# Kernel tuning notes

Measured on AMD Instinct MI355X. Metric: run time of the kernel, lower is better.

Reference implementation:

```python
import jax, jax.numpy as jnp
import numpy as np
import math

B, H, N, D = 4, 8, 2048, 64


def setup_inputs() -> dict:
    key = jax.random.key(0)
    kq, kk, kv = jax.random.split(key, 3)
    q = jax.random.normal(kq, (B, H, N, D), dtype=jnp.float32)
    k = jax.random.normal(kk, (B, H, N, D), dtype=jnp.float32)
    v = jax.random.normal(kv, (B, H, N, D), dtype=jnp.float32)
    return {"q": q, "k": k, "v": v}


def reference(q, k, v):
    # global_attention_Sub: expanded squared L2 distance ||q_i - k_j||^2
    # = qq_i - 2 q_i.k_j + kk_j, then softmax(-dist/sqrt(D)) @ v.
    scale = math.sqrt(q.shape[-1])
    inner = -2.0 * jnp.einsum('bhnd,bhmd->bhnm', q, k)          # [B,H,N,N]
    qq = jnp.sum(q * q, axis=-1, keepdims=True)                  # [B,H,N,1]
    kk = jnp.sum(k * k, axis=-1, keepdims=True)                  # [B,H,N,1]
    diff_sq = qq + inner + jnp.swapaxes(kk, -1, -2)              # [B,H,N,N]
    attn = jax.nn.softmax(-diff_sq / scale, axis=-1)
    x = jnp.einsum('bhnm,bhmd->bhnd', attn, v)                   # [B,H,N,D]
    return jnp.transpose(x, (0, 2, 1, 3))                        # [B,N,H,D]
```

## Files before the change

kernel.cpp:

```cpp
#include <hip/hip_runtime.h>

typedef __bf16 bf16x4 __attribute__((ext_vector_type(4)));
typedef __bf16 bf16x8 __attribute__((ext_vector_type(8)));
typedef float floatx4 __attribute__((ext_vector_type(4)));

constexpr int Bc = 4, Hc = 8, Nc = 2048, Dc = 64;
constexpr int BQ = 128;
constexpr int WQ = 32;
constexpr int TK = 64;
constexpr int NT = Nc / TK;
constexpr int SPS = 72;
constexpr float LOG2E = 1.44269504088896340736f;

constexpr size_t KSW_OFF = 0;
constexpr size_t VSW_OFF = (size_t)32 * NT * 8192;
constexpr size_t KKN_OFF = VSW_OFF * 2;

typedef __attribute__((address_space(1))) const unsigned int gu32;
typedef __attribute__((address_space(3))) unsigned int lu32;
__device__ __forceinline__ void dma16(const void* g, void* l) {
    __builtin_amdgcn_global_load_lds((gu32*)g, (lu32*)l, 16, 0, 0);
}
__device__ __forceinline__ void dma4(const void* g, void* l) {
    __builtin_amdgcn_global_load_lds((gu32*)g, (lu32*)l, 4, 0, 0);
}

__global__ __launch_bounds__(256) void prep_kernel(
    const float* __restrict__ Kg, const float* __restrict__ Vg, char* __restrict__ ws)
{
    __shared__ float sT[64 * 68];
    const int tid = threadIdx.x;
    const int jt = blockIdx.x, bh = blockIdx.y;

    __bf16* Ksw = (__bf16*)(ws + KSW_OFF) + ((size_t)bh * NT + jt) * 4096;
    __bf16* Vsw = (__bf16*)(ws + VSW_OFF) + ((size_t)bh * NT + jt) * 4096;
    float*  kkn = (float*)(ws + KKN_OFF) + (size_t)bh * Nc + jt * 64;
    const size_t tb = ((size_t)bh * Nc + jt * 64) * Dc;

#pragma unroll
    for (int cc = 0; cc < 2; ++cc) {
        const int g   = tid + cc * 256;
        const int key = g >> 3, kcx = g & 7;
        const int kc  = kcx ^ (key & 7);
        const float* src = Kg + tb + key * 64 + kc * 8;
        float4 a = *(const float4*)src;
        float4 b = *(const float4*)(src + 4);
        float ss = a.x*a.x + a.y*a.y + a.z*a.z + a.w*a.w
                 + b.x*b.x + b.y*b.y + b.z*b.z + b.w*b.w;
        ss += __shfl_xor(ss, 1);
        ss += __shfl_xor(ss, 2);
        ss += __shfl_xor(ss, 4);
        if (kcx == 0) kkn[key] = -(ss * 0.125f * LOG2E);
        bf16x8 c8;
        c8[0]=(__bf16)a.x; c8[1]=(__bf16)a.y; c8[2]=(__bf16)a.z; c8[3]=(__bf16)a.w;
        c8[4]=(__bf16)b.x; c8[5]=(__bf16)b.y; c8[6]=(__bf16)b.z; c8[7]=(__bf16)b.w;
        *(bf16x8*)(Ksw + g * 8) = c8;
    }
    {
        const int js = tid >> 2, dc = (tid & 3) * 16;
        const float* vr = Vg + tb + js * 64 + dc;
        float* dst = &sT[js * 68 + dc];
        *(float4*)dst       = *(const float4*)vr;
        *(float4*)(dst + 4) = *(const float4*)(vr + 4);
        *(float4*)(dst + 8) = *(const float4*)(vr + 8);
        *(float4*)(dst + 12)= *(const float4*)(vr + 12);
    }
    __syncthreads();
#pragma unroll
    for (int cc = 0; cc < 2; ++cc) {
        const int g = tid + cc * 256;
        const int d = g >> 3, kcx = g & 7;
        const int kc = kcx ^ (d & 7);
        bf16x8 c8;
#pragma unroll
        for (int e = 0; e < 8; ++e) {
            const int ee = (e + kcx) & 7;
            c8[ee] = (__bf16)sT[(kc * 8 + ee) * 68 + d];
        }
        *(bf16x8*)(Vsw + g * 8) = c8;
    }
}

__global__ __launch_bounds__(256, 2) void attn_kernel(
    const float* __restrict__ Qg, const char* __restrict__ ws, float* __restrict__ Og)
{
    __shared__ __align__(16) __bf16 sK[2][4096];
    __shared__ __align__(16) __bf16 sVall[3 * 4096];
    __shared__ __align__(16) float  skk[2][64];
    __shared__ __align__(16) __bf16 sP[BQ * SPS];
    __shared__ __align__(16) float  sl[BQ];

    const int tid  = threadIdx.x;
    const int wave = tid >> 6;
    const int lane = tid & 63;
    const int qd   = lane >> 4;
    const int c    = lane & 15;

    const int qt = blockIdx.x;
    const int bh = blockIdx.y;

    const char* Kimg = ws + KSW_OFF + (size_t)bh * NT * 8192;
    const char* Vimg = ws + VSW_OFF + (size_t)bh * NT * 8192;
    const float* kkp = (const float*)(ws + KKN_OFF) + (size_t)bh * Nc;

    const float qscale = 0.25f * LOG2E;
    const int i0 = qt * BQ + wave * WQ;

    bf16x8 qf[2][2];
#pragma unroll
    for (int h = 0; h < 2; ++h) {
        const float* qrow = Qg + ((size_t)bh * Nc + i0 + h * 16 + c) * Dc + qd * 8;
#pragma unroll
        for (int ks = 0; ks < 2; ++ks) {
            float4 a = *(const float4*)(qrow + ks * 32);
            float4 b = *(const float4*)(qrow + ks * 32 + 4);
            bf16x8 f;
            f[0] = (__bf16)(a.x * qscale); f[1] = (__bf16)(a.y * qscale);
            f[2] = (__bf16)(a.z * qscale); f[3] = (__bf16)(a.w * qscale);
            f[4] = (__bf16)(b.x * qscale); f[5] = (__bf16)(b.y * qscale);
            f[6] = (__bf16)(b.z * qscale); f[7] = (__bf16)(b.w * qscale);
            qf[h][ks] = f;
        }
    }

    const int koff0 = c * 64 + ((qd ^ (c & 7)) << 3);
    const int koff1 = c * 64 + (((4 + qd) ^ (c & 7)) << 3);

    floatx4 oacc[2][4];
#pragma unroll
    for (int h = 0; h < 2; ++h)
#pragma unroll
        for (int dt = 0; dt < 4; ++dt)
#pragma unroll
            for (int e = 0; e < 4; ++e) oacc[h][dt][e] = 0.f;
    float lp[2] = {0.f, 0.f};

    __bf16* vprev = &sVall[2 * 4096];
    __bf16* vcur  = &sVall[0];
    __bf16* vnext = &sVall[1 * 4096];

    auto stage = [&](int jt2, int kb, __bf16* vdst) {
        const char* ki = Kimg + (size_t)jt2 * 8192;
        const char* vi = Vimg + (size_t)jt2 * 8192;
#pragma unroll
        for (int i = 0; i < 2; ++i) {
            const int off    = wave * 2048 + i * 1024 + lane * 16;
            const int ldsoff = wave * 2048 + i * 1024;
            dma16(ki + off, (char*)&sK[kb][0] + ldsoff);
            dma16(vi + off, (char*)vdst + ldsoff);
        }
        if (wave == 3) dma4(kkp + jt2 * 64 + lane, &skk[kb][0]);
    };

    stage(0, 0, vcur);

    bf16x8 pfp[2][2];

    for (int jt = 0; jt < NT; ++jt) {
        const int b = jt & 1;
        __syncthreads();
        if (jt + 1 < NT) stage(jt + 1, b ^ 1, vnext);

        floatx4 st[2][4];
#pragma unroll
        for (int kt = 0; kt < 4; ++kt) {
            floatx4 kkf = *(const floatx4*)&skk[b][kt * 16 + qd * 4];
            st[0][kt] = kkf; st[1][kt] = kkf;
        }
#pragma unroll
        for (int kt = 0; kt < 4; ++kt) {
            const __bf16* kbase = &sK[b][kt * 1024];
            bf16x8 kf0 = *(const bf16x8*)(kbase + koff0);
            bf16x8 kf1 = *(const bf16x8*)(kbase + koff1);
            st[0][kt] = __builtin_amdgcn_mfma_f32_16x16x32_bf16(kf0, qf[0][0], st[0][kt], 0, 0, 0);
            st[0][kt] = __builtin_amdgcn_mfma_f32_16x16x32_bf16(kf1, qf[0][1], st[0][kt], 0, 0, 0);
            st[1][kt] = __builtin_amdgcn_mfma_f32_16x16x32_bf16(kf0, qf[1][0], st[1][kt], 0, 0, 0);
            st[1][kt] = __builtin_amdgcn_mfma_f32_16x16x32_bf16(kf1, qf[1][1], st[1][kt], 0, 0, 0);
        }

        if (jt > 0) {
#pragma unroll
            for (int dt = 0; dt < 4; ++dt) {
                const __bf16* vbase = vprev + dt * 1024;
                bf16x8 vf0 = *(const bf16x8*)(vbase + koff0);
                bf16x8 vf1 = *(const bf16x8*)(vbase + koff1);
                oacc[0][dt] = __builtin_amdgcn_mfma_f32_16x16x32_bf16(pfp[0][0], vf0, oacc[0][dt], 0, 0, 0);
                oacc[0][dt] = __builtin_amdgcn_mfma_f32_16x16x32_bf16(pfp[0][1], vf1, oacc[0][dt], 0, 0, 0);
                oacc[1][dt] = __builtin_amdgcn_mfma_f32_16x16x32_bf16(pfp[1][0], vf0, oacc[1][dt], 0, 0, 0);
                oacc[1][dt] = __builtin_amdgcn_mfma_f32_16x16x32_bf16(pfp[1][1], vf1, oacc[1][dt], 0, 0, 0);
            }
        }

#pragma unroll
        for (int h = 0; h < 2; ++h) {
            const int prow = wave * WQ + h * 16 + c;
#pragma unroll
            for (int kt = 0; kt < 4; ++kt) {
                float p0 = __builtin_amdgcn_exp2f(st[h][kt][0]);
                float p1 = __builtin_amdgcn_exp2f(st[h][kt][1]);
                float p2 = __builtin_amdgcn_exp2f(st[h][kt][2]);
                float p3 = __builtin_amdgcn_exp2f(st[h][kt][3]);
                lp[h] += (p0 + p1) + (p2 + p3);
                bf16x4 pk;
                pk[0] = (__bf16)p0; pk[1] = (__bf16)p1;
                pk[2] = (__bf16)p2; pk[3] = (__bf16)p3;
                *(bf16x4*)&sP[prow * SPS + kt * 16 + qd * 4] = pk;
            }
        }
#pragma unroll
        for (int h = 0; h < 2; ++h)
#pragma unroll
            for (int ks = 0; ks < 2; ++ks)
                pfp[h][ks] = *(const bf16x8*)&sP[(wave * WQ + h * 16 + c) * SPS + ks * 32 + qd * 8];

        __bf16* t = vprev; vprev = vcur; vcur = vnext; vnext = t;
    }

#pragma unroll
    for (int dt = 0; dt < 4; ++dt) {
        const __bf16* vbase = vprev + dt * 1024;
        bf16x8 vf0 = *(const bf16x8*)(vbase + koff0);
        bf16x8 vf1 = *(const bf16x8*)(vbase + koff1);
        oacc[0][dt] = __builtin_amdgcn_mfma_f32_16x16x32_bf16(pfp[0][0], vf0, oacc[0][dt], 0, 0, 0);
        oacc[0][dt] = __builtin_amdgcn_mfma_f32_16x16x32_bf16(pfp[0][1], vf1, oacc[0][dt], 0, 0, 0);
        oacc[1][dt] = __builtin_amdgcn_mfma_f32_16x16x32_bf16(pfp[1][0], vf0, oacc[1][dt], 0, 0, 0);
        oacc[1][dt] = __builtin_amdgcn_mfma_f32_16x16x32_bf16(pfp[1][1], vf1, oacc[1][dt], 0, 0, 0);
    }

#pragma unroll
    for (int h = 0; h < 2; ++h) {
        float l = lp[h];
        l += __shfl_xor(l, 16);
        l += __shfl_xor(l, 32);
        if (qd == 0) sl[wave * WQ + h * 16 + c] = l;
    }
    const int b_ = bh >> 3, hh = bh & 7;
#pragma unroll
    for (int h = 0; h < 2; ++h) {
        floatx4 lf = *(const floatx4*)&sl[wave * WQ + h * 16 + qd * 4];
#pragma unroll
        for (int r = 0; r < 4; ++r) {
            const float inv = 1.f / lf[r];
            const int i = i0 + h * 16 + qd * 4 + r;
            float* orow = Og + (((size_t)b_ * Nc + i) * Hc + hh) * Dc + c;
#pragma unroll
            for (int dt = 0; dt < 4; ++dt)
                orow[dt * 16] = oacc[h][dt][r] * inv;
        }
    }
}

extern "C" void kernel_launch(void* const* d_in, const int* in_sizes, int n_in,
                              void* d_out, int out_size, void* d_ws, size_t ws_size,
                              hipStream_t stream) {
    const float* q = (const float*)d_in[0];
    const float* k = (const float*)d_in[1];
    const float* v = (const float*)d_in[2];
    float* out = (float*)d_out;
    char* ws = (char*)d_ws;
    prep_kernel<<<dim3(NT, Bc * Hc), 256, 0, stream>>>(k, v, ws);
    attn_kernel<<<dim3(Nc / BQ, Bc * Hc), 256, 0, stream>>>(q, ws, out);
}
```

Baseline: 138.4 us.

## Split query block across eight waves of sixteen rows each

Doubles threads per block to 512 and gives each wave 16 query rows instead of 32, halving per-wave accumulator and Q fragment registers. Staging is rewritten so each thread issues one DMA per K/V tile. The intent is more resident waves per CU to hide LDS and DMA latency. The trade-off is that each K/V fragment read from LDS now feeds half as many MFMAs, and block-wide barriers span more waves.

Measured after the change: 136.9 us. No clear change (-1.1%).

```diff
diff --git a/kernel.cpp b/kernel.cpp
--- a/kernel.cpp
+++ b/kernel.cpp
@@ -6,7 +6,7 @@
 
 constexpr int Bc = 4, Hc = 8, Nc = 2048, Dc = 64;
 constexpr int BQ = 128;
-constexpr int WQ = 32;
+constexpr int WQ = 16;
 constexpr int TK = 64;
 constexpr int NT = Nc / TK;
 constexpr int SPS = 72;
@@ -81,7 +81,7 @@
     }
 }
 
-__global__ __launch_bounds__(256, 2) void attn_kernel(
+__global__ __launch_bounds__(512, 4) void attn_kernel(
     const float* __restrict__ Qg, const char* __restrict__ ws, float* __restrict__ Og)
 {
     __shared__ __align__(16) __bf16 sK[2][4096];
@@ -106,10 +106,9 @@
     const float qscale = 0.25f * LOG2E;
     const int i0 = qt * BQ + wave * WQ;
 
-    bf16x8 qf[2][2];
-#pragma unroll
-    for (int h = 0; h < 2; ++h) {
-        const float* qrow = Qg + ((size_t)bh * Nc + i0 + h * 16 + c) * Dc + qd * 8;
+    bf16x8 qf[2];
+    {
+        const float* qrow = Qg + ((size_t)bh * Nc + i0 + c) * Dc + qd * 8;
 #pragma unroll
         for (int ks = 0; ks < 2; ++ks) {
             float4 a = *(const float4*)(qrow + ks * 32);
@@ -119,21 +118,19 @@
             f[2] = (__bf16)(a.z * qscale); f[3] = (__bf16)(a.w * qscale);
             f[4] = (__bf16)(b.x * qscale); f[5] = (__bf16)(b.y * qscale);
             f[6] = (__bf16)(b.z * qscale); f[7] = (__bf16)(b.w * qscale);
-            qf[h][ks] = f;
+            qf[ks] = f;
         }
     }
 
     const int koff0 = c * 64 + ((qd ^ (c & 7)) << 3);
     const int koff1 = c * 64 + (((4 + qd) ^ (c & 7)) << 3);
 
-    floatx4 oacc[2][4];
-#pragma unroll
-    for (int h = 0; h < 2; ++h)
-#pragma unroll
-        for (int dt = 0; dt < 4; ++dt)
-#pragma unroll
-            for (int e = 0; e < 4; ++e) oacc[h][dt][e] = 0.f;
-    float lp[2] = {0.f, 0.f};
+    floatx4 oacc[4];
+#pragma unroll
+    for (int dt = 0; dt < 4; ++dt)
+#pragma unroll
+        for (int e = 0; e < 4; ++e) oacc[dt][e] = 0.f;
+    float lp = 0.f;
 
     __bf16* vprev = &sVall[2 * 4096];
     __bf16* vcur  = &sVall[0];
@@ -142,40 +139,32 @@
     auto stage = [&](int jt2, int kb, __bf16* vdst) {
         const char* ki = Kimg + (size_t)jt2 * 8192;
         const char* vi = Vimg + (size_t)jt2 * 8192;
-#pragma unroll
-        for (int i = 0; i < 2; ++i) {
-            const int off    = wave * 2048 + i * 1024 + lane * 16;
-            const int ldsoff = wave * 2048 + i * 1024;
-            dma16(ki + off, (char*)&sK[kb][0] + ldsoff);
-            dma16(vi + off, (char*)vdst + ldsoff);
-        }
-        if (wave == 3) dma4(kkp + jt2 * 64 + lane, &skk[kb][0]);
+        const int off = tid * 16;
+        dma16(ki + off, (char*)&sK[kb][0] + off);
+        dma16(vi + off, (char*)vdst + off);
+        if (wave == 7) dma4(kkp + jt2 * 64 + lane, &skk[kb][0]);
     };
 
     stage(0, 0, vcur);
 
-    bf16x8 pfp[2][2];
+    bf16x8 pfp[2];
 
     for (int jt = 0; jt < NT; ++jt) {
         const int b = jt & 1;
         __syncthreads();
         if (jt + 1 < NT) stage(jt + 1, b ^ 1, vnext);
 
-        floatx4 st[2][4];
-#pragma unroll
-        for (int kt = 0; kt < 4; ++kt) {
-            floatx4 kkf = *(const floatx4*)&skk[b][kt * 16 + qd * 4];
-            st[0][kt] = kkf; st[1][kt] = kkf;
-        }
+        floatx4 st[4];
+#pragma unroll
+        for (int kt = 0; kt < 4; ++kt)
+            st[kt] = *(const floatx4*)&skk[b][kt * 16 + qd * 4];
 #pragma unroll
         for (int kt = 0; kt < 4; ++kt) {
             const __bf16* kbase = &sK[b][kt * 1024];
             bf16x8 kf0 = *(const bf16x8*)(kbase + koff0);
             bf16x8 kf1 = *(const bf16x8*)(kbase + koff1);
-            st[0][kt] = __builtin_amdgcn_mfma_f32_16x16x32_bf16(kf0, qf[0][0], st[0][kt], 0, 0, 0);
-            st[0][kt] = __builtin_amdgcn_mfma_f32_16x16x32_bf16(kf1, qf[0][1], st[0][kt], 0, 0, 0);
-            st[1][kt] = __builtin_amdgcn_mfma_f32_16x16x32_bf16(kf0, qf[1][0], st[1][kt], 0, 0, 0);
-            st[1][kt] = __builtin_amdgcn_mfma_f32_16x16x32_bf16(kf1, qf[1][1], st[1][kt], 0, 0, 0);
+            st[kt] = __builtin_amdgcn_mfma_f32_16x16x32_bf16(kf0, qf[0], st[kt], 0, 0, 0);
+            st[kt] = __builtin_amdgcn_mfma_f32_16x16x32_bf16(kf1, qf[1], st[kt], 0, 0, 0);
         }
 
         if (jt > 0) {
@@ -184,23 +173,20 @@
                 const __bf16* vbase = vprev + dt * 1024;
                 bf16x8 vf0 = *(const bf16x8*)(vbase + koff0);
                 bf16x8 vf1 = *(const bf16x8*)(vbase + koff1);
-                oacc[0][dt] = __builtin_amdgcn_mfma_f32_16x16x32_bf16(pfp[0][0], vf0, oacc[0][dt], 0, 0, 0);
-                oacc[0][dt] = __builtin_amdgcn_mfma_f32_16x16x32_bf16(pfp[0][1], vf1, oacc[0][dt], 0, 0, 0);
-                oacc[1][dt] = __builtin_amdgcn_mfma_f32_16x16x32_bf16(pfp[1][0], vf0, oacc[1][dt], 0, 0, 0);
-                oacc[1][dt] = __builtin_amdgcn_mfma_f32_16x16x32_bf16(pfp[1][1], vf1, oacc[1][dt], 0, 0, 0);
+                oacc[dt] = __builtin_amdgcn_mfma_f32_16x16x32_bf16(pfp[0], vf0, oacc[dt], 0, 0, 0);
+                oacc[dt] = __builtin_amdgcn_mfma_f32_16x16x32_bf16(pfp[1], vf1, oacc[dt], 0, 0, 0);
             }
         }
 
-#pragma unroll
-        for (int h = 0; h < 2; ++h) {
-            const int prow = wave * WQ + h * 16 + c;
+        {
+            const int prow = wave * WQ + c;
 #pragma unroll
             for (int kt = 0; kt < 4; ++kt) {
-                float p0 = __builtin_amdgcn_exp2f(st[h][kt][0]);
-                float p1 = __builtin_amdgcn_exp2f(st[h][kt][1]);
-                float p2 = __builtin_amdgcn_exp2f(st[h][kt][2]);
-                float p3 = __builtin_amdgcn_exp2f(st[h][kt][3]);
-                lp[h] += (p0 + p1) + (p2 + p3);
+                float p0 = __builtin_amdgcn_exp2f(st[kt][0]);
+                float p1 = __builtin_amdgcn_exp2f(st[kt][1]);
+                float p2 = __builtin_amdgcn_exp2f(st[kt][2]);
+                float p3 = __builtin_amdgcn_exp2f(st[kt][3]);
+                lp += (p0 + p1) + (p2 + p3);
                 bf16x4 pk;
                 pk[0] = (__bf16)p0; pk[1] = (__bf16)p1;
                 pk[2] = (__bf16)p2; pk[3] = (__bf16)p3;
@@ -208,10 +194,8 @@
             }
         }
 #pragma unroll
-        for (int h = 0; h < 2; ++h)
-#pragma unroll
-            for (int ks = 0; ks < 2; ++ks)
-                pfp[h][ks] = *(const bf16x8*)&sP[(wave * WQ + h * 16 + c) * SPS + ks * 32 + qd * 8];
+        for (int ks = 0; ks < 2; ++ks)
+            pfp[ks] = *(const bf16x8*)&sP[(wave * WQ + c) * SPS + ks * 32 + qd * 8];
 
         __bf16* t = vprev; vprev = vcur; vcur = vnext; vnext = t;
     }
@@ -221,31 +205,27 @@
         const __bf16* vbase = vprev + dt * 1024;
         bf16x8 vf0 = *(const bf16x8*)(vbase + koff0);
         bf16x8 vf1 = *(const bf16x8*)(vbase + koff1);
-        oacc[0][dt] = __builtin_amdgcn_mfma_f32_16x16x32_bf16(pfp[0][0], vf0, oacc[0][dt], 0, 0, 0);
-        oacc[0][dt] = __builtin_amdgcn_mfma_f32_16x16x32_bf16(pfp[0][1], vf1, oacc[0][dt], 0, 0, 0);
-        oacc[1][dt] = __builtin_amdgcn_mfma_f32_16x16x32_bf16(pfp[1][0], vf0, oacc[1][dt], 0, 0, 0);
-        oacc[1][dt] = __builtin_amdgcn_mfma_f32_16x16x32_bf16(pfp[1][1], vf1, oacc[1][dt], 0, 0, 0);
-    }
-
-#pragma unroll
-    for (int h = 0; h < 2; ++h) {
-        float l = lp[h];
+        oacc[dt] = __builtin_amdgcn_mfma_f32_16x16x32_bf16(pfp[0], vf0, oacc[dt], 0, 0, 0);
+        oacc[dt] = __builtin_amdgcn_mfma_f32_16x16x32_bf16(pfp[1], vf1, oacc[dt], 0, 0, 0);
+    }
+
+    {
+        float l = lp;
         l += __shfl_xor(l, 16);
         l += __shfl_xor(l, 32);
-        if (qd == 0) sl[wave * WQ + h * 16 + c] = l;
+        if (qd == 0) sl[wave * WQ + c] = l;
     }
     const int b_ = bh >> 3, hh = bh & 7;
-#pragma unroll
-    for (int h = 0; h < 2; ++h) {
-        floatx4 lf = *(const floatx4*)&sl[wave * WQ + h * 16 + qd * 4];
+    {
+        floatx4 lf = *(const floatx4*)&sl[wave * WQ + qd * 4];
 #pragma unroll
         for (int r = 0; r < 4; ++r) {
             const float inv = 1.f / lf[r];
-            const int i = i0 + h * 16 + qd * 4 + r;
+            const int i = i0 + qd * 4 + r;
             float* orow = Og + (((size_t)b_ * Nc + i) * Hc + hh) * Dc + c;
 #pragma unroll
             for (int dt = 0; dt < 4; ++dt)
-                orow[dt * 16] = oacc[h][dt][r] * inv;
+                orow[dt * 16] = oacc[dt][r] * inv;
         }
     }
 }
@@ -259,5 +239,5 @@
     float* out = (float*)d_out;
     char* ws = (char*)d_ws;
     prep_kernel<<<dim3(NT, Bc * Hc), 256, 0, stream>>>(k, v, ws);
-    attn_kernel<<<dim3(Nc / BQ, Bc * Hc), 256, 0, stream>>>(q, ws, out);
-}
+    attn_kernel<<<dim3(Nc / BQ, Bc * Hc), 512, 0, stream>>>(q, ws, out);
+}
```
